# Performance work log

Hardware: AMD Instinct MI355X
Metric: run time of the kernel (lower is better)

The kernel has to match this reference:

```python
import jax, jax.numpy as jnp
import numpy as np

N, E, F_IN, HID, NC = 8192, 262144, 128, 64, 10
EPS_BN = 1e-5


def gat_layer(x, edge_src, edge_dst, W, att_src, att_dst, bias, heads):
    # x: [N, Fin]; W: [Fin, heads*C]; att_*: [heads, C]; bias: [C]
    n = x.shape[0]
    h = (x @ W).reshape(n, heads, -1)                     # [N,H,C]
    a_s = (h * att_src).sum(-1)                           # [N,H]
    a_d = (h * att_dst).sum(-1)                           # [N,H]
    e = jax.nn.leaky_relu(a_s[edge_src] + a_d[edge_dst], 0.2)  # [E,H]
    # segment softmax over destination node (self-loops guarantee >=1 edge per dst)
    m = jax.ops.segment_max(e, edge_dst, num_segments=n)
    ex = jnp.exp(e - m[edge_dst])
    s = jax.ops.segment_sum(ex, edge_dst, num_segments=n)
    alpha = ex / (s[edge_dst] + 1e-16)                    # [E,H]
    out = jax.ops.segment_sum(h[edge_src] * alpha[:, :, None], edge_dst, num_segments=n)  # [N,H,C]
    return out.mean(axis=1) + bias                        # concat=False -> mean over heads


def batch_norm(x, gamma, beta):
    mu = x.mean(axis=0)
    var = x.var(axis=0)  # biased, as PyTorch uses for normalization
    return (x - mu) * jax.lax.rsqrt(var + EPS_BN) * gamma + beta


def mha(x, Wq, Wk, Wv, bq, bk, bv, Wo, bo, num_heads=4):
    n, d = x.shape
    hd = d // num_heads
    q = (x @ Wq.T + bq).reshape(n, num_heads, hd)
    k = (x @ Wk.T + bk).reshape(n, num_heads, hd)
    v = (x @ Wv.T + bv).reshape(n, num_heads, hd)
    scores = jnp.einsum('nhd,mhd->hnm', q, k) / jnp.sqrt(jnp.asarray(hd, x.dtype))
    attn = jax.nn.softmax(scores, axis=-1)
    out = jnp.einsum('hnm,mhd->nhd', attn, v).reshape(n, d)
    return out @ Wo.T + bo


def setup_inputs() -> dict:
    key = jax.random.key(0)
    ks = jax.random.split(key, 32)
    d = {}
    d['x'] = jax.random.normal(ks[0], (N, F_IN), dtype=jnp.float32)
    d['edge_index'] = jax.random.randint(ks[1], (2, E), 0, N, dtype=jnp.int32)
    heads_list = [8, 8, 1]
    fins = [F_IN, HID, HID]
    for i, (fin, h) in enumerate(zip(fins, heads_list)):
        sc = 1.0 / np.sqrt(fin)
        d[f'W{i}'] = jax.random.normal(ks[2 + 4 * i], (fin, h * HID), dtype=jnp.float32) * sc
        d[f'as{i}'] = jax.random.normal(ks[3 + 4 * i], (h, HID), dtype=jnp.float32) * 0.1
        d[f'ad{i}'] = jax.random.normal(ks[4 + 4 * i], (h, HID), dtype=jnp.float32) * 0.1
        d[f'b{i}'] = jnp.zeros((HID,), dtype=jnp.float32)
    d['bn_gamma'] = jnp.ones((3, HID), dtype=jnp.float32)
    d['bn_beta'] = jnp.zeros((3, HID), dtype=jnp.float32)
    sc = 1.0 / np.sqrt(HID)
    for j, name in enumerate(['Wq', 'Wk', 'Wv', 'Wo']):
        d[name] = jax.random.normal(ks[16 + j], (HID, HID), dtype=jnp.float32) * sc
    for name in ['bq', 'bk', 'bv', 'bo']:
        d[name] = jnp.zeros((HID,), dtype=jnp.float32)
    d['Wc1'] = jax.random.normal(ks[20], (HID // 2, HID), dtype=jnp.float32) * sc
    d['bc1'] = jnp.zeros((HID // 2,), dtype=jnp.float32)
    d['Wc2'] = jax.random.normal(ks[21], (NC, HID // 2), dtype=jnp.float32) * (1.0 / np.sqrt(HID // 2))
    d['bc2'] = jnp.zeros((NC,), dtype=jnp.float32)
    return d


def reference(x, edge_index, W0, as0, ad0, b0, W1, as1, ad1, b1, W2, as2, ad2, b2,
              bn_gamma, bn_beta, Wq, Wk, Wv, bq, bk, bv, Wo, bo, Wc1, bc1, Wc2, bc2):
    n = x.shape[0]
    # PyG GATConv default add_self_loops=True
    loops = jnp.arange(n, dtype=edge_index.dtype)
    src = jnp.concatenate([edge_index[0], loops])
    dst = jnp.concatenate([edge_index[1], loops])
    heads_list = [8, 8, 1]
    params = [(W0, as0, ad0, b0), (W1, as1, ad1, b1), (W2, as2, ad2, b2)]
    for i in range(3):
        Wl, asl, adl, bl = params[i]
        x = gat_layer(x, src, dst, Wl, asl, adl, bl, heads_list[i])
        x = batch_norm(x, bn_gamma[i], bn_beta[i])
        x = jax.nn.relu(x)  # dropout inactive (eval)
    x = mha(x, Wq, Wk, Wv, bq, bk, bv, Wo, bo)
    x = jax.nn.relu(x @ Wc1.T + bc1)
    return x @ Wc2.T + bc2
```

## Files before the change

### kernel.cpp

```cpp
#include <hip/hip_runtime.h>
#include <hip/hip_bf16.h>

#define NN 8192
#define EE 262144
#define HID 64

typedef _Float16 half4_t __attribute__((ext_vector_type(4)));
typedef _Float16 half8_t __attribute__((ext_vector_type(8)));
typedef float f32x4 __attribute__((ext_vector_type(4)));

extern "C" __device__ float __ocml_native_exp2_f32(float);
#define EXP2N(x) __ocml_native_exp2_f32(x)

template<bool TRANS_B, int ACT>
__global__ void gemm_f32(const float* __restrict__ A, const float* __restrict__ B,
                         const float* __restrict__ bias, float* __restrict__ C,
                         int M, int Nc, int K) {
    __shared__ float As[16][65];
    __shared__ float Bs[16][65];
    int tid = threadIdx.x;
    int brow = blockIdx.y * 64, bcol = blockIdx.x * 64;
    int tr = (tid / 16) * 4;
    int tc = (tid % 16) * 4;
    float acc[4][4] = {};
    for (int k0 = 0; k0 < K; k0 += 16) {
        {
            int r  = tid / 4;
            int kk = (tid % 4) * 4;
            const float* a = A + (size_t)(brow + r) * K + k0 + kk;
            #pragma unroll
            for (int j = 0; j < 4; ++j) As[kk + j][r] = a[j];
        }
        if (!TRANS_B) {
            int kk = tid / 16;
            int n4 = (tid % 16) * 4;
            #pragma unroll
            for (int j = 0; j < 4; ++j) {
                int n = bcol + n4 + j;
                Bs[kk][n4 + j] = (n < Nc) ? B[(size_t)(k0 + kk) * Nc + n] : 0.f;
            }
        } else {
            int n  = tid / 4;
            int kk = (tid % 4) * 4;
            #pragma unroll
            for (int j = 0; j < 4; ++j)
                Bs[kk + j][n] = (bcol + n < Nc) ? B[(size_t)(bcol + n) * K + k0 + kk + j] : 0.f;
        }
        __syncthreads();
        #pragma unroll
        for (int kk = 0; kk < 16; ++kk) {
            float av[4], bv[4];
            #pragma unroll
            for (int i = 0; i < 4; ++i) av[i] = As[kk][tr + i];
            #pragma unroll
            for (int j = 0; j < 4; ++j) bv[j] = Bs[kk][tc + j];
            #pragma unroll
            for (int i = 0; i < 4; ++i)
                #pragma unroll
                for (int j = 0; j < 4; ++j)
                    acc[i][j] += av[i] * bv[j];
        }
        __syncthreads();
    }
    #pragma unroll
    for (int i = 0; i < 4; ++i) {
        int r = brow + tr + i;
        #pragma unroll
        for (int j = 0; j < 4; ++j) {
            int c = bcol + tc + j;
            if (c < Nc) {
                float v = acc[i][j];
                if (bias) v += bias[c];
                if (ACT == 1) v = fmaxf(v, 0.f);
                C[(size_t)r * Nc + c] = v;
            }
        }
    }
}

template<bool TRANS_B, bool OUT_F16, int ACT, bool GAT>
__device__ __forceinline__ void mfma_gemm_body(
        const float* __restrict__ A, const float* __restrict__ B,
        const float* __restrict__ bias, void* __restrict__ Cout,
        int M, int Nc, int K, float scale, int brow, int bcol,
        const float* __restrict__ att_s, const float* __restrict__ att_d,
        float* __restrict__ a_s, float* __restrict__ a_d, int H) {
    __shared__ _Float16 Ah[64][36];
    __shared__ _Float16 Bt[64][36];
    int tid  = threadIdx.x;
    int wave = tid >> 6, lane = tid & 63, lo16 = lane & 15, g = lane >> 4;
    f32x4 acc[4];
    #pragma unroll
    for (int i = 0; i < 4; ++i) acc[i] = (f32x4){0.f, 0.f, 0.f, 0.f};

    for (int k0 = 0; k0 < K; k0 += 32) {
        {
            int r  = tid >> 2;
            int ks = (tid & 3) * 8;
            const float* ap = A + (size_t)(brow + r) * K + k0 + ks;
            f32x4 a0 = *(const f32x4*)ap;
            f32x4 a1 = *(const f32x4*)(ap + 4);
            half4_t h0, h1;
            #pragma unroll
            for (int i = 0; i < 4; ++i) { h0[i] = (_Float16)a0[i]; h1[i] = (_Float16)a1[i]; }
            *(half4_t*)&Ah[r][ks]     = h0;
            *(half4_t*)&Ah[r][ks + 4] = h1;
        }
        if (TRANS_B) {
            int n  = tid >> 2;
            int ks = (tid & 3) * 8;
            const float* bp = B + (size_t)(bcol + n) * K + k0 + ks;
            f32x4 b0 = *(const f32x4*)bp;
            f32x4 b1 = *(const f32x4*)(bp + 4);
            half4_t h0, h1;
            #pragma unroll
            for (int i = 0; i < 4; ++i) { h0[i] = (_Float16)b0[i]; h1[i] = (_Float16)b1[i]; }
            *(half4_t*)&Bt[n][ks]     = h0;
            *(half4_t*)&Bt[n][ks + 4] = h1;
        } else {
            int n  = tid & 63;
            int kb = (tid >> 6) * 8;
            half4_t h0, h1;
            #pragma unroll
            for (int i = 0; i < 4; ++i)
                h0[i] = (_Float16)B[(size_t)(k0 + kb + i) * Nc + bcol + n];
            #pragma unroll
            for (int i = 0; i < 4; ++i)
                h1[i] = (_Float16)B[(size_t)(k0 + kb + 4 + i) * Nc + bcol + n];
            *(half4_t*)&Bt[n][kb]     = h0;
            *(half4_t*)&Bt[n][kb + 4] = h1;
        }
        __syncthreads();
        #pragma unroll
        for (int kh = 0; kh < 2; ++kh) {
            half4_t af = *(const half4_t*)&Ah[wave * 16 + lo16][kh * 16 + g * 4];
            #pragma unroll
            for (int cf = 0; cf < 4; ++cf) {
                half4_t bf = *(const half4_t*)&Bt[cf * 16 + lo16][kh * 16 + g * 4];
                acc[cf] = __builtin_amdgcn_mfma_f32_16x16x16f16(af, bf, acc[cf], 0, 0, 0);
            }
        }
        __syncthreads();
    }
    int rbase = brow + wave * 16 + g * 4;
    #pragma unroll
    for (int cf = 0; cf < 4; ++cf) {
        int c = bcol + cf * 16 + lo16;
        float bv = bias ? bias[c] : 0.f;
        #pragma unroll
        for (int reg = 0; reg < 4; ++reg) {
            float v = (acc[cf][reg] + bv) * scale;
            if (ACT == 1) v = fmaxf(v, 0.f);
            if (OUT_F16) ((_Float16*)Cout)[(size_t)(rbase + reg) * Nc + c] = (_Float16)v;
            else         ((float*)Cout)[(size_t)(rbase + reg) * Nc + c] = v;
        }
    }
    if (GAT) {
        float as_c[4], ad_c[4];
        #pragma unroll
        for (int cf = 0; cf < 4; ++cf) {
            int c = bcol + cf * 16 + lo16;
            as_c[cf] = att_s[c];
            ad_c[cf] = att_d[c];
        }
        int head = bcol >> 6;
        #pragma unroll
        for (int reg = 0; reg < 4; ++reg) {
            float ps = 0.f, pd = 0.f;
            #pragma unroll
            for (int cf = 0; cf < 4; ++cf) {
                ps += acc[cf][reg] * as_c[cf];
                pd += acc[cf][reg] * ad_c[cf];
            }
            #pragma unroll
            for (int off = 8; off; off >>= 1) {
                ps += __shfl_xor(ps, off);
                pd += __shfl_xor(pd, off);
            }
            if (lo16 == 0) {
                int row = rbase + reg;
                a_s[row * H + head] = ps;
                a_d[row * H + head] = pd;
            }
        }
    }
}

template<bool TRANS_B, bool OUT_F16, int ACT, bool GAT>
__global__ void mfma_gemm(const float* __restrict__ A, const float* __restrict__ B,
                          const float* __restrict__ bias, void* __restrict__ Cout,
                          int M, int Nc, int K, float scale,
                          const float* __restrict__ att_s, const float* __restrict__ att_d,
                          float* __restrict__ a_s, float* __restrict__ a_d, int H) {
    mfma_gemm_body<TRANS_B, OUT_F16, ACT, GAT>(A, B, bias, Cout, M, Nc, K, scale,
                                               blockIdx.y * 64, blockIdx.x * 64,
                                               att_s, att_d, a_s, a_d, H);
}

__global__ void qkv_gemm(const float* __restrict__ A,
                         const float* __restrict__ Wq, const float* __restrict__ Wk,
                         const float* __restrict__ Wv, const float* __restrict__ bq,
                         const float* __restrict__ bk, const float* __restrict__ bv,
                         _Float16* __restrict__ qh, _Float16* __restrict__ kh,
                         _Float16* __restrict__ vh, int M, float qscale) {
    int z = blockIdx.z;
    const float* B    = z == 0 ? Wq : (z == 1 ? Wk : Wv);
    const float* bias = z == 0 ? bq : (z == 1 ? bk : bv);
    _Float16* Cout    = z == 0 ? qh : (z == 1 ? kh : vh);
    float scale       = z == 0 ? qscale : 1.f;
    mfma_gemm_body<true, true, 0, false>(A, B, bias, Cout, M, 64, 64, scale,
                                         blockIdx.y * 64, 0,
                                         nullptr, nullptr, nullptr, nullptr, 0);
}

__global__ void count_deg(const int* __restrict__ ei, int* __restrict__ deg, int E) {
    int e = blockIdx.x * 256 + threadIdx.x;
    if (e < E) atomicAdd(&deg[ei[E + e]], 1);
}

__global__ void scan_deg(const int* __restrict__ deg, int* __restrict__ row_ptr,
                         int* __restrict__ cursor, int N) {
    __shared__ int tmp[1024];
    int tid = threadIdx.x;
    int base = tid * 8;
    int local[8];
    int s = 0;
    #pragma unroll
    for (int j = 0; j < 8; ++j) { local[j] = deg[base + j] + 1; s += local[j]; }
    tmp[tid] = s;
    __syncthreads();
    for (int off = 1; off < 1024; off <<= 1) {
        int add = (tid >= off) ? tmp[tid - off] : 0;
        __syncthreads();
        tmp[tid] += add;
        __syncthreads();
    }
    int run = tmp[tid] - s;
    #pragma unroll
    for (int j = 0; j < 8; ++j) {
        row_ptr[base + j] = run;
        cursor[base + j]  = run;
        run += local[j];
    }
    if (tid == 1023) row_ptr[N] = run;
}

__global__ void fill_csr(const int* __restrict__ ei, int* __restrict__ cursor,
                         int* __restrict__ col, int E, int N) {
    int e = blockIdx.x * 256 + threadIdx.x;
    if (e < E) {
        int dst = ei[E + e];
        int pos = atomicAdd(&cursor[dst], 1);
        col[pos] = ei[e];
    } else if (e < E + N) {
        int n = e - E;
        int pos = atomicAdd(&cursor[n], 1);
        col[pos] = n;
    }
}

__global__ void gat_gather_h8(const _Float16* __restrict__ h, const float* __restrict__ a_s,
                              const float* __restrict__ a_d, const int* __restrict__ row_ptr,
                              const int* __restrict__ col, float* __restrict__ out, int N) {
    __shared__ float wsf[4][64][8];
    __shared__ int   wsc[4][64];
    int t = threadIdx.x, wave = t >> 6, lane = t & 63;
    int n = (blockIdx.x * 256 + t) >> 6;
    int hd = lane >> 3;
    int beg = row_ptr[n], end = row_ptr[n + 1];
    float ad[8];
    #pragma unroll
    for (int i = 0; i < 8; ++i) ad[i] = a_d[n * 8 + i];
    float m[8];
    #pragma unroll
    for (int i = 0; i < 8; ++i) m[i] = -1e30f;
    for (int j = beg + lane; j < end; j += 64) {
        int c = col[j];
        f32x4 s0 = *(const f32x4*)(a_s + (size_t)c * 8);
        f32x4 s1 = *(const f32x4*)(a_s + (size_t)c * 8 + 4);
        #pragma unroll
        for (int i = 0; i < 4; ++i) {
            float sa = s0[i] + ad[i];
            sa = sa > 0.f ? sa : 0.2f * sa;
            m[i] = fmaxf(m[i], sa);
            float sb = s1[i] + ad[4 + i];
            sb = sb > 0.f ? sb : 0.2f * sb;
            m[4 + i] = fmaxf(m[4 + i], sb);
        }
    }
    #pragma unroll
    for (int i = 0; i < 8; ++i)
        #pragma unroll
        for (int off = 32; off; off >>= 1) m[i] = fmaxf(m[i], __shfl_xor(m[i], off));
    const _Float16* hb = h + (size_t)lane * 8;
    float acc[8] = {0.f, 0.f, 0.f, 0.f, 0.f, 0.f, 0.f, 0.f};
    float den[8] = {0.f, 0.f, 0.f, 0.f, 0.f, 0.f, 0.f, 0.f};
    for (int base = beg; base < end; base += 64) {
        int j = base + lane;
        int cj = 0;
        float w[8];
        #pragma unroll
        for (int i = 0; i < 8; ++i) w[i] = 0.f;
        if (j < end) {
            cj = col[j];
            f32x4 s0 = *(const f32x4*)(a_s + (size_t)cj * 8);
            f32x4 s1 = *(const f32x4*)(a_s + (size_t)cj * 8 + 4);
            #pragma unroll
            for (int i = 0; i < 4; ++i) {
                float sa = s0[i] + ad[i];
                sa = sa > 0.f ? sa : 0.2f * sa;
                w[i] = __expf(sa - m[i]);
                den[i] += w[i];
                float sb = s1[i] + ad[4 + i];
                sb = sb > 0.f ? sb : 0.2f * sb;
                w[4 + i] = __expf(sb - m[4 + i]);
                den[4 + i] += w[4 + i];
            }
        }
        wsc[wave][lane] = cj;
        *(f32x4*)&wsf[wave][lane][0] = (f32x4){w[0], w[1], w[2], w[3]};
        *(f32x4*)&wsf[wave][lane][4] = (f32x4){w[4], w[5], w[6], w[7]};
        int cnt = min(64, end - base);
        #pragma unroll 2
        for (int k = 0; k < cnt; ++k) {
            int ck  = wsc[wave][k];
            float wk = wsf[wave][k][hd];
            half8_t hv = *(const half8_t*)(hb + (size_t)ck * 512);
            #pragma unroll
            for (int i = 0; i < 8; ++i) acc[i] += wk * (float)hv[i];
        }
    }
    #pragma unroll
    for (int i = 0; i < 8; ++i)
        #pragma unroll
        for (int off = 32; off; off >>= 1) den[i] += __shfl_xor(den[i], off);
    float inv = 1.f / ((den[hd] + 1e-16f) * 8.f);
    float y[8];
    #pragma unroll
    for (int i = 0; i < 8; ++i) y[i] = acc[i] * inv;
    #pragma unroll
    for (int i = 0; i < 8; ++i) {
        y[i] += __shfl_xor(y[i], 8);
        y[i] += __shfl_xor(y[i], 16);
        y[i] += __shfl_xor(y[i], 32);
    }
    if (lane < 8) {
        *(f32x4*)(out + (size_t)n * 64 + lane * 8)     = (f32x4){y[0], y[1], y[2], y[3]};
        *(f32x4*)(out + (size_t)n * 64 + lane * 8 + 4) = (f32x4){y[4], y[5], y[6], y[7]};
    }
}

__global__ void gat_gather3(const _Float16* __restrict__ h, const float* __restrict__ a_s,
                            const float* __restrict__ a_d, const int* __restrict__ row_ptr,
                            const int* __restrict__ col, float* __restrict__ out,
                            int N, int H) {
    __shared__ uint2 wc[4][64];
    int t    = threadIdx.x;
    int wave = t >> 6;
    int lane = t & 63;
    int wid  = (blockIdx.x * 256 + t) >> 6;
    if (wid >= N * H) return;
    int n = wid / H, hh = wid % H;
    int beg = row_ptr[n], end = row_ptr[n + 1];
    float adn = a_d[n * H + hh];
    float m = -1e30f;
    for (int j = beg + lane; j < end; j += 64) {
        float sc = a_s[col[j] * H + hh] + adn;
        sc = sc > 0.f ? sc : 0.2f * sc;
        m = fmaxf(m, sc);
    }
    #pragma unroll
    for (int off = 32; off; off >>= 1) m = fmaxf(m, __shfl_xor(m, off));
    const _Float16* hb = h + (size_t)hh * 64 + lane;
    const size_t rs = (size_t)H * 64;
    float denom = 0.f;
    float acc0 = 0.f, acc1 = 0.f, acc2 = 0.f, acc3 = 0.f;
    float acc4 = 0.f, acc5 = 0.f, acc6 = 0.f, acc7 = 0.f;
    for (int base = beg; base < end; base += 64) {
        int j = base + lane;
        float w = 0.f; int s = 0;
        if (j < end) {
            s = col[j];
            float sc = a_s[s * H + hh] + adn;
            sc = sc > 0.f ? sc : 0.2f * sc;
            w = __expf(sc - m);
        }
        denom += w;
        uint2 p; p.x = __float_as_uint(w); p.y = (unsigned)s;
        wc[wave][lane] = p;
        int cnt = min(64, end - base);
        int k = 0;
        for (; k + 8 <= cnt; k += 8) {
            uint2 p0 = wc[wave][k];
            uint2 p1 = wc[wave][k + 1];
            uint2 p2 = wc[wave][k + 2];
            uint2 p3 = wc[wave][k + 3];
            uint2 p4 = wc[wave][k + 4];
            uint2 p5 = wc[wave][k + 5];
            uint2 p6 = wc[wave][k + 6];
            uint2 p7 = wc[wave][k + 7];
            acc0 += __uint_as_float(p0.x) * (float)hb[(size_t)p0.y * rs];
            acc1 += __uint_as_float(p1.x) * (float)hb[(size_t)p1.y * rs];
            acc2 += __uint_as_float(p2.x) * (float)hb[(size_t)p2.y * rs];
            acc3 += __uint_as_float(p3.x) * (float)hb[(size_t)p3.y * rs];
            acc4 += __uint_as_float(p4.x) * (float)hb[(size_t)p4.y * rs];
            acc5 += __uint_as_float(p5.x) * (float)hb[(size_t)p5.y * rs];
            acc6 += __uint_as_float(p6.x) * (float)hb[(size_t)p6.y * rs];
            acc7 += __uint_as_float(p7.x) * (float)hb[(size_t)p7.y * rs];
        }
        for (; k < cnt; ++k) {
            uint2 p0 = wc[wave][k];
            acc0 += __uint_as_float(p0.x) * (float)hb[(size_t)p0.y * rs];
        }
    }
    float acc = ((acc0 + acc1) + (acc2 + acc3)) + ((acc4 + acc5) + (acc6 + acc7));
    #pragma unroll
    for (int off = 32; off; off >>= 1) denom += __shfl_xor(denom, off);
    atomicAdd(&out[n * 64 + lane], acc / ((denom + 1e-16f) * H));
}

__global__ void bn_stats(const float* __restrict__ x, const float* __restrict__ gamma,
                         const float* __restrict__ beta, float* __restrict__ scale,
                         float* __restrict__ shift, int N) {
    int c = blockIdx.x;
    float s = 0.f, ss = 0.f;
    for (int r = threadIdx.x; r < N; r += 256) {
        float v = x[(size_t)r * 64 + c];
        s += v; ss += v * v;
    }
    #pragma unroll
    for (int off = 32; off; off >>= 1) {
        s  += __shfl_xor(s, off);
        ss += __shfl_xor(ss, off);
    }
    __shared__ float red[8];
    int wv = threadIdx.x >> 6, ln = threadIdx.x & 63;
    if (ln == 0) { red[wv] = s; red[4 + wv] = ss; }
    __syncthreads();
    if (threadIdx.x == 0) {
        float S  = red[0] + red[1] + red[2] + red[3];
        float SS = red[4] + red[5] + red[6] + red[7];
        float mu  = S / N;
        float var = SS / N - mu * mu;
        float istd = rsqrtf(var + 1e-5f);
        scale[c] = gamma[c] * istd;
        shift[c] = beta[c] - mu * gamma[c] * istd;
    }
}

__global__ void bn_apply(const float* x, const float* __restrict__ scale,
                         const float* __restrict__ shift, float* __restrict__ y,
                         float* xz, int total) {
    int i = blockIdx.x * 256 + threadIdx.x;
    if (i < total) {
        int c = i & 63;
        float v = x[i];
        y[i] = fmaxf(v * scale[c] + shift[c], 0.f);
        xz[i] = 0.f;
    }
}

__global__ void vkpack(const _Float16* __restrict__ vh, const _Float16* __restrict__ kh,
                       _Float16* __restrict__ vt, _Float16* __restrict__ khp, int N) {
    __shared__ _Float16 tile[64][68];
    int kb = blockIdx.x * 64;
    int t  = threadIdx.x;
    {
        int r = t >> 2, c0 = (t & 3) * 16;
        half8_t x0 = *(const half8_t*)(vh + (size_t)(kb + r) * 64 + c0);
        half8_t x1 = *(const half8_t*)(vh + (size_t)(kb + r) * 64 + c0 + 8);
        #pragma unroll
        for (int i = 0; i < 8; ++i) { tile[r][c0 + i] = x0[i]; tile[r][c0 + 8 + i] = x1[i]; }
    }
    #pragma unroll
    for (int rep = 0; rep < 2; ++rep) {
        int l = t + 256 * rep;
        int n = kb + (l >> 3), c8 = (l & 7) * 8;
        half8_t v = *(const half8_t*)(kh + (size_t)n * 64 + c8);
        *(half8_t*)(khp + ((size_t)(c8 >> 4) * N + n) * 16 + (c8 & 15)) = v;
    }
    __syncthreads();
    {
        int c = t >> 2, ks = (t & 3) * 16;
        half8_t y0, y1;
        #pragma unroll
        for (int i = 0; i < 8; ++i) { y0[i] = tile[ks + i][c]; y1[i] = tile[ks + 8 + i][c]; }
        *(half8_t*)(vt + (size_t)c * N + kb + ks)     = y0;
        *(half8_t*)(vt + (size_t)c * N + kb + ks + 8) = y1;
    }
}

__global__ __launch_bounds__(512) void mha_fa5(const _Float16* __restrict__ qh,
                                               const _Float16* __restrict__ khp,
                                               const _Float16* __restrict__ vt,
                                               float* __restrict__ ao, int N) {
    __shared__ alignas(16) char smem[38912];
    typedef _Float16 (*KtT)[2][64][20];
    typedef _Float16 (*VtT)[2][16][68];
    KtT Kt = (KtT)smem;
    VtT Vt = (VtT)(smem + 20480);
    float* MBp = (float*)(smem + 37888);
    float* OBp = (float*)smem;

    int h    = blockIdx.y;
    int t    = threadIdx.x;
    int lane = t & 63;
    int wave = t >> 6;
    int grp  = wave >> 1;
    int wsub = wave & 1;
    int lo16 = lane & 15;
    int g    = lane >> 4;
    int q    = blockIdx.x * 32 + wsub * 16 + lo16;

    half4_t qf = *(const half4_t*)(qh + (size_t)q * 64 + h * 16 + g * 4);
    const _Float16* kp = khp + (size_t)h * N * 16;
    const _Float16* vp = vt + (size_t)h * 16 * N;

    int gt   = t & 127;
    int skey = gt >> 1, sch = (gt & 1) * 8;
    int sd   = gt >> 3, skv = (gt & 7) * 8;

    {
        int kt = grp * 64;
        half8_t kv = *(const half8_t*)(kp + (size_t)(kt + skey) * 16 + sch);
        half8_t vv = *(const half8_t*)(vp + (size_t)sd * N + kt + skv);
        half4_t a, b, c, d;
        #pragma unroll
        for (int i = 0; i < 4; ++i) { a[i] = kv[i]; b[i] = kv[4 + i]; c[i] = vv[i]; d[i] = vv[4 + i]; }
        *(half4_t*)&Kt[grp][0][skey][sch]     = a;
        *(half4_t*)&Kt[grp][0][skey][sch + 4] = b;
        *(half4_t*)&Vt[grp][0][sd][skv]       = c;
        *(half4_t*)&Vt[grp][0][sd][skv + 4]   = d;
    }

    float m = -1e30f, l = 0.f;
    f32x4 o = {0.f, 0.f, 0.f, 0.f};
    const f32x4 zero = {0.f, 0.f, 0.f, 0.f};
    const int nit = N / 256;

    for (int it = 0; it < nit; ++it) {
        int cur = it & 1;
        __syncthreads();
        if (it + 1 < nit) {
            int kt = ((it + 1) * 4 + grp) * 64;
            half8_t kv = *(const half8_t*)(kp + (size_t)(kt + skey) * 16 + sch);
            half8_t vv = *(const half8_t*)(vp + (size_t)sd * N + kt + skv);
            half4_t a, b, c, d;
            #pragma unroll
            for (int i = 0; i < 4; ++i) { a[i] = kv[i]; b[i] = kv[4 + i]; c[i] = vv[i]; d[i] = vv[4 + i]; }
            *(half4_t*)&Kt[grp][cur ^ 1][skey][sch]     = a;
            *(half4_t*)&Kt[grp][cur ^ 1][skey][sch + 4] = b;
            *(half4_t*)&Vt[grp][cur ^ 1][sd][skv]       = c;
            *(half4_t*)&Vt[grp][cur ^ 1][sd][skv + 4]   = d;
        }
        f32x4 s[4];
        __builtin_amdgcn_s_setprio(1);
        #pragma unroll
        for (int st = 0; st < 4; ++st) {
            half4_t kf = *(const half4_t*)&Kt[grp][cur][st * 16 + lo16][g * 4];
            s[st] = __builtin_amdgcn_mfma_f32_16x16x16f16(kf, qf, zero, 0, 0, 0);
        }
        __builtin_amdgcn_s_setprio(0);
        float t0 = fmaxf(fmaxf(s[0][0], s[0][1]), s[0][2]);
        float t1 = fmaxf(fmaxf(s[0][3], s[1][0]), s[1][1]);
        float t2 = fmaxf(fmaxf(s[1][2], s[1][3]), s[2][0]);
        float t3 = fmaxf(fmaxf(s[2][1], s[2][2]), s[2][3]);
        float t4 = fmaxf(fmaxf(s[3][0], s[3][1]), fmaxf(s[3][2], s[3][3]));
        float tm = fmaxf(fmaxf(fmaxf(t0, t1), fmaxf(t2, t3)), t4);
        tm = fmaxf(tm, __shfl_xor(tm, 16));
        tm = fmaxf(tm, __shfl_xor(tm, 32));
        if (!__all(tm <= m + 8.f)) {
            float mnew = fmaxf(m, tm);
            float r = EXP2N(m - mnew);
            l *= r;
            #pragma unroll
            for (int i = 0; i < 4; ++i) o[i] *= r;
            m = mnew;
        }
        float lsum = 0.f;
        half4_t pf[4];
        #pragma unroll
        for (int st = 0; st < 4; ++st) {
            float p0 = EXP2N(s[st][0] - m);
            float p1 = EXP2N(s[st][1] - m);
            float p2 = EXP2N(s[st][2] - m);
            float p3 = EXP2N(s[st][3] - m);
            lsum += (p0 + p1) + (p2 + p3);
            auto lo = __builtin_amdgcn_cvt_pkrtz(p0, p1);
            auto hi = __builtin_amdgcn_cvt_pkrtz(p2, p3);
            pf[st][0] = (_Float16)lo[0]; pf[st][1] = (_Float16)lo[1];
            pf[st][2] = (_Float16)hi[0]; pf[st][3] = (_Float16)hi[1];
        }
        l += lsum;
        __builtin_amdgcn_s_setprio(1);
        #pragma unroll
        for (int st = 0; st < 4; ++st) {
            half4_t vf = *(const half4_t*)&Vt[grp][cur][lo16][st * 16 + g * 4];
            o = __builtin_amdgcn_mfma_f32_16x16x16f16(vf, pf[st], o, 0, 0, 0);
        }
        __builtin_amdgcn_s_setprio(0);
    }
    l += __shfl_xor(l, 16);
    l += __shfl_xor(l, 32);

    __syncthreads();
    if (grp != 0) {
        if (lane < 16) {
            MBp[((wsub * 4 + grp) * 2 + 0) * 16 + lane] = m;
            MBp[((wsub * 4 + grp) * 2 + 1) * 16 + lane] = l;
        }
        #pragma unroll
        for (int i = 0; i < 4; ++i)
            OBp[((wsub * 4 + grp) * 16 + g * 4 + i) * 17 + lo16] = o[i];
    }
    __syncthreads();
    if (grp == 0) {
        float M = m, L = l;
        f32x4 O = o;
        #pragma unroll
        for (int gg = 1; gg < 4; ++gg) {
            float m1 = MBp[((wsub * 4 + gg) * 2 + 0) * 16 + lo16];
            float l1 = MBp[((wsub * 4 + gg) * 2 + 1) * 16 + lo16];
            float Mn = fmaxf(M, m1);
            float e0 = EXP2N(M - Mn), e1 = EXP2N(m1 - Mn);
            L = L * e0 + l1 * e1;
            #pragma unroll
            for (int i = 0; i < 4; ++i)
                O[i] = O[i] * e0 + OBp[((wsub * 4 + gg) * 16 + g * 4 + i) * 17 + lo16] * e1;
            M = Mn;
        }
        float inv = 1.f / L;
        f32x4 res;
        #pragma unroll
        for (int i = 0; i < 4; ++i) res[i] = O[i] * inv;
        *(f32x4*)(ao + (size_t)q * 64 + h * 16 + g * 4) = res;
    }
}

static inline void launch_gemm(const float* A, const float* B, const float* bias, float* C,
                               int M, int Nc, int K, bool transB, int act, hipStream_t st) {
    dim3 grid((Nc + 63) / 64, M / 64), blk(256);
    if (!transB)       gemm_f32<false, 0><<<grid, blk, 0, st>>>(A, B, bias, C, M, Nc, K);
    else if (act == 0) gemm_f32<true, 0><<<grid, blk, 0, st>>>(A, B, bias, C, M, Nc, K);
    else               gemm_f32<true, 1><<<grid, blk, 0, st>>>(A, B, bias, C, M, Nc, K);
}

extern "C" void kernel_launch(void* const* d_in, const int* in_sizes, int n_in,
                              void* d_out, int out_size, void* d_ws, size_t ws_size,
                              hipStream_t stream) {
    const int N = NN, E = EE;
    const float* x    = (const float*)d_in[0];
    const int*   ei   = (const int*)d_in[1];
    const float* W[3]   = {(const float*)d_in[2], (const float*)d_in[6], (const float*)d_in[10]};
    const float* as_[3] = {(const float*)d_in[3], (const float*)d_in[7], (const float*)d_in[11]};
    const float* ad_[3] = {(const float*)d_in[4], (const float*)d_in[8], (const float*)d_in[12]};
    const float* bn_g = (const float*)d_in[14];
    const float* bn_b = (const float*)d_in[15];
    const float* Wq = (const float*)d_in[16];
    const float* Wk = (const float*)d_in[17];
    const float* Wv = (const float*)d_in[18];
    const float* Wo = (const float*)d_in[19];
    const float* bq = (const float*)d_in[20];
    const float* bk = (const float*)d_in[21];
    const float* bv = (const float*)d_in[22];
    const float* bo = (const float*)d_in[23];
    const float* Wc1 = (const float*)d_in[24];
    const float* bc1 = (const float*)d_in[25];
    const float* Wc2 = (const float*)d_in[26];
    const float* bc2 = (const float*)d_in[27];

    char* ws = (char*)d_ws;
    _Float16* h16 = (_Float16*)(ws + 0);
    _Float16* qh = (_Float16*)(ws + 9437184);
    _Float16* kh = (_Float16*)(ws + 10485760);
    _Float16* vh = (_Float16*)(ws + 11534336);
    _Float16* vt = (_Float16*)(ws + 12582912);
    _Float16* khp = (_Float16*)(ws + 13631488);
    float* a_s  = (float*)(ws + 16777216);
    float* a_d  = (float*)(ws + 17039360);
    int* row_ptr = (int*)(ws + 17301504);
    int* cursor  = (int*)(ws + 17334528);
    int* deg     = (int*)(ws + 17367296);
    int* col     = (int*)(ws + 17400064);
    float* xg   = (float*)(ws + 18481408);
    float* xb   = (float*)(ws + 20578560);
    float* ao   = (float*)(ws + 28967168);
    float* c1   = (float*)(ws + 31064320);
    float* bnscale = (float*)(ws + 32112896);
    float* bnshift = bnscale + 64;

    hipMemsetAsync(deg, 0, (size_t)N * 4, stream);
    count_deg<<<(E + 255) / 256, 256, 0, stream>>>(ei, deg, E);
    scan_deg<<<1, 1024, 0, stream>>>(deg, row_ptr, cursor, N);
    fill_csr<<<(E + N + 255) / 256, 256, 0, stream>>>(ei, cursor, col, E, N);

    const int heads[3] = {8, 8, 1};
    const int fins[3]  = {128, 64, 64};
    const float* xin = x;
    for (int i = 0; i < 3; ++i) {
        int H = heads[i], K = fins[i];
        mfma_gemm<false, true, 0, true><<<dim3(H, N / 64), 256, 0, stream>>>(
            xin, W[i], nullptr, h16, N, H * 64, K, 1.f, as_[i], ad_[i], a_s, a_d, H);
        if (H == 8)
            gat_gather_h8<<<N / 4, 256, 0, stream>>>(h16, a_s, a_d, row_ptr, col, xg, N);
        else
            gat_gather3<<<(N * H) / 4, 256, 0, stream>>>(h16, a_s, a_d, row_ptr, col, xg, N, H);
        bn_stats<<<64, 256, 0, stream>>>(xg, bn_g + i * 64, bn_b + i * 64, bnscale, bnshift, N);
        bn_apply<<<(N * 64) / 256, 256, 0, stream>>>(xg, bnscale, bnshift, xb, xg, N * 64);
        xin = xb;
    }

    qkv_gemm<<<dim3(1, N / 64, 3), 256, 0, stream>>>(
        xb, Wq, Wk, Wv, bq, bk, bv, qh, kh, vh, N, 0.36067376f);
    vkpack<<<N / 64, 256, 0, stream>>>(vh, kh, vt, khp, N);
    mha_fa5<<<dim3(N / 32, 4), 512, 0, stream>>>(qh, khp, vt, ao, N);
    mfma_gemm<true, false, 0, false><<<dim3(1, N / 64), 256, 0, stream>>>(
        ao, Wo, bo, xg, N, 64, 64, 1.f, nullptr, nullptr, nullptr, nullptr, 0);

    launch_gemm(xg, Wc1, bc1, c1, N, 32, 64, true, 1, stream);
    launch_gemm(c1, Wc2, bc2, (float*)d_out, N, 10, 32, true, 0, stream);
}
```

Before: 300.1 us.

## Fuse batch-norm apply into next GEMM loads and merge output MLP head

Removes the separate bn_apply pass by applying BN scale/shift and ReLU while loading the A tile in the following GAT or QKV GEMM. Replaces the Wo projection and the two classifier GEMMs with a single mlp_head kernel that keeps intermediates in shared memory and uses fp16 MFMA. Specializes the single-head gather to write outputs directly instead of accumulating with atomics. This saves launches and full-activation round trips. It no longer zeroes the gather output buffers between layers, so it depends on how the 8-head gather writes its results.

```diff
diff --git a/kernel.cpp b/kernel.cpp
--- a/kernel.cpp
+++ b/kernel.cpp
@@ -12,79 +12,16 @@
 extern "C" __device__ float __ocml_native_exp2_f32(float);
 #define EXP2N(x) __ocml_native_exp2_f32(x)
 
-template<bool TRANS_B, int ACT>
-__global__ void gemm_f32(const float* __restrict__ A, const float* __restrict__ B,
-                         const float* __restrict__ bias, float* __restrict__ C,
-                         int M, int Nc, int K) {
-    __shared__ float As[16][65];
-    __shared__ float Bs[16][65];
-    int tid = threadIdx.x;
-    int brow = blockIdx.y * 64, bcol = blockIdx.x * 64;
-    int tr = (tid / 16) * 4;
-    int tc = (tid % 16) * 4;
-    float acc[4][4] = {};
-    for (int k0 = 0; k0 < K; k0 += 16) {
-        {
-            int r  = tid / 4;
-            int kk = (tid % 4) * 4;
-            const float* a = A + (size_t)(brow + r) * K + k0 + kk;
-            #pragma unroll
-            for (int j = 0; j < 4; ++j) As[kk + j][r] = a[j];
-        }
-        if (!TRANS_B) {
-            int kk = tid / 16;
-            int n4 = (tid % 16) * 4;
-            #pragma unroll
-            for (int j = 0; j < 4; ++j) {
-                int n = bcol + n4 + j;
-                Bs[kk][n4 + j] = (n < Nc) ? B[(size_t)(k0 + kk) * Nc + n] : 0.f;
-            }
-        } else {
-            int n  = tid / 4;
-            int kk = (tid % 4) * 4;
-            #pragma unroll
-            for (int j = 0; j < 4; ++j)
-                Bs[kk + j][n] = (bcol + n < Nc) ? B[(size_t)(bcol + n) * K + k0 + kk + j] : 0.f;
-        }
-        __syncthreads();
-        #pragma unroll
-        for (int kk = 0; kk < 16; ++kk) {
-            float av[4], bv[4];
-            #pragma unroll
-            for (int i = 0; i < 4; ++i) av[i] = As[kk][tr + i];
-            #pragma unroll
-            for (int j = 0; j < 4; ++j) bv[j] = Bs[kk][tc + j];
-            #pragma unroll
-            for (int i = 0; i < 4; ++i)
-                #pragma unroll
-                for (int j = 0; j < 4; ++j)
-                    acc[i][j] += av[i] * bv[j];
-        }
-        __syncthreads();
-    }
-    #pragma unroll
-    for (int i = 0; i < 4; ++i) {
-        int r = brow + tr + i;
-        #pragma unroll
-        for (int j = 0; j < 4; ++j) {
-            int c = bcol + tc + j;
-            if (c < Nc) {
-                float v = acc[i][j];
-                if (bias) v += bias[c];
-                if (ACT == 1) v = fmaxf(v, 0.f);
-                C[(size_t)r * Nc + c] = v;
-            }
-        }
-    }
-}
-
-template<bool TRANS_B, bool OUT_F16, int ACT, bool GAT>
+#define MFMA16(a, b, c) __builtin_amdgcn_mfma_f32_16x16x16f16(a, b, c, 0, 0, 0)
+
+template<bool TRANS_B, bool OUT_F16, int ACT, bool GAT, bool BN>
 __device__ __forceinline__ void mfma_gemm_body(
         const float* __restrict__ A, const float* __restrict__ B,
         const float* __restrict__ bias, void* __restrict__ Cout,
         int M, int Nc, int K, float scale, int brow, int bcol,
         const float* __restrict__ att_s, const float* __restrict__ att_d,
-        float* __restrict__ a_s, float* __restrict__ a_d, int H) {
+        float* __restrict__ a_s, float* __restrict__ a_d, int H,
+        const float* __restrict__ bnsc, const float* __restrict__ bnsh) {
     __shared__ _Float16 Ah[64][36];
     __shared__ _Float16 Bt[64][36];
     int tid  = threadIdx.x;
@@ -100,6 +37,14 @@
             const float* ap = A + (size_t)(brow + r) * K + k0 + ks;
             f32x4 a0 = *(const f32x4*)ap;
             f32x4 a1 = *(const f32x4*)(ap + 4);
+            if (BN) {
+                #pragma unroll
+                for (int i = 0; i < 4; ++i) {
+                    int c0 = k0 + ks + i, c1 = c0 + 4;
+                    a0[i] = fmaxf(a0[i] * bnsc[c0] + bnsh[c0], 0.f);
+                    a1[i] = fmaxf(a1[i] * bnsc[c1] + bnsh[c1], 0.f);
+                }
+            }
             half4_t h0, h1;
             #pragma unroll
             for (int i = 0; i < 4; ++i) { h0[i] = (_Float16)a0[i]; h1[i] = (_Float16)a1[i]; }
@@ -137,7 +82,7 @@
             #pragma unroll
             for (int cf = 0; cf < 4; ++cf) {
                 half4_t bf = *(const half4_t*)&Bt[cf * 16 + lo16][kh * 16 + g * 4];
-                acc[cf] = __builtin_amdgcn_mfma_f32_16x16x16f16(af, bf, acc[cf], 0, 0, 0);
+                acc[cf] = MFMA16(af, bf, acc[cf]);
             }
         }
         __syncthreads();
@@ -186,15 +131,16 @@
     }
 }
 
-template<bool TRANS_B, bool OUT_F16, int ACT, bool GAT>
+template<bool TRANS_B, bool OUT_F16, int ACT, bool GAT, bool BN>
 __global__ void mfma_gemm(const float* __restrict__ A, const float* __restrict__ B,
                           const float* __restrict__ bias, void* __restrict__ Cout,
                           int M, int Nc, int K, float scale,
                           const float* __restrict__ att_s, const float* __restrict__ att_d,
-                          float* __restrict__ a_s, float* __restrict__ a_d, int H) {
-    mfma_gemm_body<TRANS_B, OUT_F16, ACT, GAT>(A, B, bias, Cout, M, Nc, K, scale,
-                                               blockIdx.y * 64, blockIdx.x * 64,
-                                               att_s, att_d, a_s, a_d, H);
+                          float* __restrict__ a_s, float* __restrict__ a_d, int H,
+                          const float* __restrict__ bnsc, const float* __restrict__ bnsh) {
+    mfma_gemm_body<TRANS_B, OUT_F16, ACT, GAT, BN>(A, B, bias, Cout, M, Nc, K, scale,
+                                                   blockIdx.y * 64, blockIdx.x * 64,
+                                                   att_s, att_d, a_s, a_d, H, bnsc, bnsh);
 }
 
 __global__ void qkv_gemm(const float* __restrict__ A,
@@ -202,15 +148,17 @@
                          const float* __restrict__ Wv, const float* __restrict__ bq,
                          const float* __restrict__ bk, const float* __restrict__ bv,
                          _Float16* __restrict__ qh, _Float16* __restrict__ kh,
-                         _Float16* __restrict__ vh, int M, float qscale) {
+                         _Float16* __restrict__ vh, int M, float qscale,
+                         const float* __restrict__ bnsc, const float* __restrict__ bnsh) {
     int z = blockIdx.z;
     const float* B    = z == 0 ? Wq : (z == 1 ? Wk : Wv);
     const float* bias = z == 0 ? bq : (z == 1 ? bk : bv);
     _Float16* Cout    = z == 0 ? qh : (z == 1 ? kh : vh);
     float scale       = z == 0 ? qscale : 1.f;
-    mfma_gemm_body<true, true, 0, false>(A, B, bias, Cout, M, 64, 64, scale,
-                                         blockIdx.y * 64, 0,
-                                         nullptr, nullptr, nullptr, nullptr, 0);
+    mfma_gemm_body<true, true, 0, false, true>(A, B, bias, Cout, M, 64, 64, scale,
+                                               blockIdx.y * 64, 0,
+                                               nullptr, nullptr, nullptr, nullptr, 0,
+                                               bnsc, bnsh);
 }
 
 __global__ void count_deg(const int* __restrict__ ei, int* __restrict__ deg, int E) {
@@ -350,29 +298,25 @@
     }
 }
 
-__global__ void gat_gather3(const _Float16* __restrict__ h, const float* __restrict__ a_s,
-                            const float* __restrict__ a_d, const int* __restrict__ row_ptr,
-                            const int* __restrict__ col, float* __restrict__ out,
-                            int N, int H) {
+__global__ void gat_gather_h1(const _Float16* __restrict__ h, const float* __restrict__ a_s,
+                              const float* __restrict__ a_d, const int* __restrict__ row_ptr,
+                              const int* __restrict__ col, float* __restrict__ out, int N) {
     __shared__ uint2 wc[4][64];
     int t    = threadIdx.x;
     int wave = t >> 6;
     int lane = t & 63;
-    int wid  = (blockIdx.x * 256 + t) >> 6;
-    if (wid >= N * H) return;
-    int n = wid / H, hh = wid % H;
+    int n    = (blockIdx.x * 256 + t) >> 6;
     int beg = row_ptr[n], end = row_ptr[n + 1];
-    float adn = a_d[n * H + hh];
+    float adn = a_d[n];
     float m = -1e30f;
     for (int j = beg + lane; j < end; j += 64) {
-        float sc = a_s[col[j] * H + hh] + adn;
+        float sc = a_s[col[j]] + adn;
         sc = sc > 0.f ? sc : 0.2f * sc;
         m = fmaxf(m, sc);
     }
     #pragma unroll
     for (int off = 32; off; off >>= 1) m = fmaxf(m, __shfl_xor(m, off));
-    const _Float16* hb = h + (size_t)hh * 64 + lane;
-    const size_t rs = (size_t)H * 64;
+    const _Float16* hb = h + lane;
     float denom = 0.f;
     float acc0 = 0.f, acc1 = 0.f, acc2 = 0.f, acc3 = 0.f;
     float acc4 = 0.f, acc5 = 0.f, acc6 = 0.f, acc7 = 0.f;
@@ -381,7 +325,7 @@
         float w = 0.f; int s = 0;
         if (j < end) {
             s = col[j];
-            float sc = a_s[s * H + hh] + adn;
+            float sc = a_s[s] + adn;
             sc = sc > 0.f ? sc : 0.2f * sc;
             w = __expf(sc - m);
         }
@@ -399,24 +343,24 @@
             uint2 p5 = wc[wave][k + 5];
             uint2 p6 = wc[wave][k + 6];
             uint2 p7 = wc[wave][k + 7];
-            acc0 += __uint_as_float(p0.x) * (float)hb[(size_t)p0.y * rs];
-            acc1 += __uint_as_float(p1.x) * (float)hb[(size_t)p1.y * rs];
-            acc2 += __uint_as_float(p2.x) * (float)hb[(size_t)p2.y * rs];
-            acc3 += __uint_as_float(p3.x) * (float)hb[(size_t)p3.y * rs];
-            acc4 += __uint_as_float(p4.x) * (float)hb[(size_t)p4.y * rs];
-            acc5 += __uint_as_float(p5.x) * (float)hb[(size_t)p5.y * rs];
-            acc6 += __uint_as_float(p6.x) * (float)hb[(size_t)p6.y * rs];
-            acc7 += __uint_as_float(p7.x) * (float)hb[(size_t)p7.y * rs];
+            acc0 += __uint_as_float(p0.x) * (float)hb[(size_t)p0.y * 64];
+            acc1 += __uint_as_float(p1.x) * (float)hb[(size_t)p1.y * 64];
+            acc2 += __uint_as_float(p2.x) * (float)hb[(size_t)p2.y * 64];
+            acc3 += __uint_as_float(p3.x) * (float)hb[(size_t)p3.y * 64];
+            acc4 += __uint_as_float(p4.x) * (float)hb[(size_t)p4.y * 64];
+            acc5 += __uint_as_float(p5.x) * (float)hb[(size_t)p5.y * 64];
+            acc6 += __uint_as_float(p6.x) * (float)hb[(size_t)p6.y * 64];
+            acc7 += __uint_as_float(p7.x) * (float)hb[(size_t)p7.y * 64];
         }
         for (; k < cnt; ++k) {
             uint2 p0 = wc[wave][k];
-            acc0 += __uint_as_float(p0.x) * (float)hb[(size_t)p0.y * rs];
+            acc0 += __uint_as_float(p0.x) * (float)hb[(size_t)p0.y * 64];
         }
     }
     float acc = ((acc0 + acc1) + (acc2 + acc3)) + ((acc4 + acc5) + (acc6 + acc7));
     #pragma unroll
     for (int off = 32; off; off >>= 1) denom += __shfl_xor(denom, off);
-    atomicAdd(&out[n * 64 + lane], acc / ((denom + 1e-16f) * H));
+    out[(size_t)n * 64 + lane] = acc / (denom + 1e-16f);
 }
 
 __global__ void bn_stats(const float* __restrict__ x, const float* __restrict__ gamma,
@@ -445,18 +389,6 @@
         float istd = rsqrtf(var + 1e-5f);
         scale[c] = gamma[c] * istd;
         shift[c] = beta[c] - mu * gamma[c] * istd;
-    }
-}
-
-__global__ void bn_apply(const float* x, const float* __restrict__ scale,
-                         const float* __restrict__ shift, float* __restrict__ y,
-                         float* xz, int total) {
-    int i = blockIdx.x * 256 + threadIdx.x;
-    if (i < total) {
-        int c = i & 63;
-        float v = x[i];
-        y[i] = fmaxf(v * scale[c] + shift[c], 0.f);
-        xz[i] = 0.f;
     }
 }
 
@@ -558,7 +490,7 @@
         #pragma unroll
         for (int st = 0; st < 4; ++st) {
             half4_t kf = *(const half4_t*)&Kt[grp][cur][st * 16 + lo16][g * 4];
-            s[st] = __builtin_amdgcn_mfma_f32_16x16x16f16(kf, qf, zero, 0, 0, 0);
+            s[st] = MFMA16(kf, qf, zero);
         }
         __builtin_amdgcn_s_setprio(0);
         float t0 = fmaxf(fmaxf(s[0][0], s[0][1]), s[0][2]);
@@ -596,7 +528,7 @@
         #pragma unroll
         for (int st = 0; st < 4; ++st) {
             half4_t vf = *(const half4_t*)&Vt[grp][cur][lo16][st * 16 + g * 4];
-            o = __builtin_amdgcn_mfma_f32_16x16x16f16(vf, pf[st], o, 0, 0, 0);
+            o = MFMA16(vf, pf[st], o);
         }
         __builtin_amdgcn_s_setprio(0);
     }
@@ -637,12 +569,122 @@
     }
 }
 
-static inline void launch_gemm(const float* A, const float* B, const float* bias, float* C,
-                               int M, int Nc, int K, bool transB, int act, hipStream_t st) {
-    dim3 grid((Nc + 63) / 64, M / 64), blk(256);
-    if (!transB)       gemm_f32<false, 0><<<grid, blk, 0, st>>>(A, B, bias, C, M, Nc, K);
-    else if (act == 0) gemm_f32<true, 0><<<grid, blk, 0, st>>>(A, B, bias, C, M, Nc, K);
-    else               gemm_f32<true, 1><<<grid, blk, 0, st>>>(A, B, bias, C, M, Nc, K);
+__global__ void mlp_head(const float* __restrict__ ao,
+                         const float* __restrict__ Wo, const float* __restrict__ bo,
+                         const float* __restrict__ Wc1, const float* __restrict__ bc1,
+                         const float* __restrict__ Wc2, const float* __restrict__ bc2,
+                         float* __restrict__ outp, int N) {
+    __shared__ _Float16 At[64][68];
+    __shared__ _Float16 Bt[64][68];
+    int t = threadIdx.x, wave = t >> 6, lane = t & 63, lo16 = lane & 15, g = lane >> 4;
+    int brow = blockIdx.x * 64;
+    const f32x4 zero = {0.f, 0.f, 0.f, 0.f};
+    {
+        int r = t >> 2, c0 = (t & 3) * 16;
+        const float* ap = ao + (size_t)(brow + r) * 64 + c0;
+        const float* wp = Wo + (size_t)r * 64 + c0;
+        #pragma unroll
+        for (int j = 0; j < 16; j += 4) {
+            f32x4 va = *(const f32x4*)(ap + j);
+            f32x4 vw = *(const f32x4*)(wp + j);
+            half4_t ha, hw;
+            #pragma unroll
+            for (int i = 0; i < 4; ++i) { ha[i] = (_Float16)va[i]; hw[i] = (_Float16)vw[i]; }
+            *(half4_t*)&At[r][c0 + j] = ha;
+            *(half4_t*)&Bt[r][c0 + j] = hw;
+        }
+    }
+    __syncthreads();
+    f32x4 acc1[4];
+    #pragma unroll
+    for (int i = 0; i < 4; ++i) acc1[i] = zero;
+    #pragma unroll
+    for (int kc = 0; kc < 4; ++kc) {
+        half4_t af = *(const half4_t*)&At[wave * 16 + lo16][kc * 16 + g * 4];
+        #pragma unroll
+        for (int cf = 0; cf < 4; ++cf) {
+            half4_t bf = *(const half4_t*)&Bt[cf * 16 + lo16][kc * 16 + g * 4];
+            acc1[cf] = MFMA16(af, bf, acc1[cf]);
+        }
+    }
+    #pragma unroll
+    for (int cf = 0; cf < 4; ++cf) {
+        int c = cf * 16 + lo16;
+        float bv = bo[c];
+        #pragma unroll
+        for (int reg = 0; reg < 4; ++reg)
+            At[wave * 16 + g * 4 + reg][c] = (_Float16)(acc1[cf][reg] + bv);
+    }
+    __syncthreads();
+    {
+        int r = t >> 2, c0 = (t & 3) * 16;
+        if (r < 32) {
+            const float* wp = Wc1 + (size_t)r * 64 + c0;
+            #pragma unroll
+            for (int j = 0; j < 16; j += 4) {
+                f32x4 vw = *(const f32x4*)(wp + j);
+                half4_t hw;
+                #pragma unroll
+                for (int i = 0; i < 4; ++i) hw[i] = (_Float16)vw[i];
+                *(half4_t*)&Bt[r][c0 + j] = hw;
+            }
+        }
+    }
+    __syncthreads();
+    f32x4 acc2[2];
+    acc2[0] = zero; acc2[1] = zero;
+    #pragma unroll
+    for (int kc = 0; kc < 4; ++kc) {
+        half4_t af = *(const half4_t*)&At[wave * 16 + lo16][kc * 16 + g * 4];
+        #pragma unroll
+        for (int cf = 0; cf < 2; ++cf) {
+            half4_t bf = *(const half4_t*)&Bt[cf * 16 + lo16][kc * 16 + g * 4];
+            acc2[cf] = MFMA16(af, bf, acc2[cf]);
+        }
+    }
+    #pragma unroll
+    for (int cf = 0; cf < 2; ++cf) {
+        int c = cf * 16 + lo16;
+        float bv = bc1[c];
+        #pragma unroll
+        for (int reg = 0; reg < 4; ++reg)
+            At[wave * 16 + g * 4 + reg][c] = (_Float16)fmaxf(acc2[cf][reg] + bv, 0.f);
+    }
+    __syncthreads();
+    {
+        if (t < 32) {
+            int r = t >> 1, c0 = (t & 1) * 16;
+            half4_t hw;
+            #pragma unroll
+            for (int j = 0; j < 16; j += 4) {
+                if (r < 10) {
+                    f32x4 vw = *(const f32x4*)(Wc2 + (size_t)r * 32 + c0 + j);
+                    #pragma unroll
+                    for (int i = 0; i < 4; ++i) hw[i] = (_Float16)vw[i];
+                } else {
+                    #pragma unroll
+                    for (int i = 0; i < 4; ++i) hw[i] = (_Float16)0.f;
+                }
+                *(half4_t*)&Bt[r][c0 + j] = hw;
+            }
+        }
+    }
+    __syncthreads();
+    f32x4 acc3 = zero;
+    #pragma unroll
+    for (int kc = 0; kc < 2; ++kc) {
+        half4_t af = *(const half4_t*)&At[wave * 16 + lo16][kc * 16 + g * 4];
+        half4_t bf = *(const half4_t*)&Bt[lo16][kc * 16 + g * 4];
+        acc3 = MFMA16(af, bf, acc3);
+    }
+    if (lo16 < 10) {
+        float bv = bc2[lo16];
+        #pragma unroll
+        for (int reg = 0; reg < 4; ++reg) {
+            int row = brow + wave * 16 + g * 4 + reg;
+            outp[(size_t)row * 10 + lo16] = acc3[reg] + bv;
+        }
+    }
 }
 
 extern "C" void kernel_launch(void* const* d_in, const int* in_sizes, int n_in,
@@ -682,10 +724,9 @@
     int* cursor  = (int*)(ws + 17334528);
     int* deg     = (int*)(ws + 17367296);
     int* col     = (int*)(ws + 17400064);
-    float* xg   = (float*)(ws + 18481408);
-    float* xb   = (float*)(ws + 20578560);
+    float* g0   = (float*)(ws + 18481408);
+    float* g1   = (float*)(ws + 20578560);
     float* ao   = (float*)(ws + 28967168);
-    float* c1   = (float*)(ws + 31064320);
     float* bnscale = (float*)(ws + 32112896);
     float* bnshift = bnscale + 64;
 
@@ -694,29 +735,23 @@
     scan_deg<<<1, 1024, 0, stream>>>(deg, row_ptr, cursor, N);
     fill_csr<<<(E + N + 255) / 256, 256, 0, stream>>>(ei, cursor, col, E, N);
 
-    const int heads[3] = {8, 8, 1};
-    const int fins[3]  = {128, 64, 64};
-    const float* xin = x;
-    for (int i = 0; i < 3; ++i) {
-        int H = heads[i], K = fins[i];
-        mfma_gemm<false, true, 0, true><<<dim3(H, N / 64), 256, 0, stream>>>(
-            xin, W[i], nullptr, h16, N, H * 64, K, 1.f, as_[i], ad_[i], a_s, a_d, H);
-        if (H == 8)
-            gat_gather_h8<<<N / 4, 256, 0, stream>>>(h16, a_s, a_d, row_ptr, col, xg, N);
-        else
-            gat_gather3<<<(N * H) / 4, 256, 0, stream>>>(h16, a_s, a_d, row_ptr, col, xg, N, H);
-        bn_stats<<<64, 256, 0, stream>>>(xg, bn_g + i * 64, bn_b + i * 64, bnscale, bnshift, N);
-        bn_apply<<<(N * 64) / 256, 256, 0, stream>>>(xg, bnscale, bnshift, xb, xg, N * 64);
-        xin = xb;
-    }
+    mfma_gemm<false, true, 0, true, false><<<dim3(8, N / 64), 256, 0, stream>>>(
+        x, W[0], nullptr, h16, N, 512, 128, 1.f, as_[0], ad_[0], a_s, a_d, 8, nullptr, nullptr);
+    gat_gather_h8<<<N / 4, 256, 0, stream>>>(h16, a_s, a_d, row_ptr, col, g0, N);
+    bn_stats<<<64, 256, 0, stream>>>(g0, bn_g, bn_b, bnscale, bnshift, N);
+    mfma_gemm<false, true, 0, true, true><<<dim3(8, N / 64), 256, 0, stream>>>(
+        g0, W[1], nullptr, h16, N, 512, 64, 1.f, as_[1], ad_[1], a_s, a_d, 8, bnscale, bnshift);
+    gat_gather_h8<<<N / 4, 256, 0, stream>>>(h16, a_s, a_d, row_ptr, col, g1, N);
+    bn_stats<<<64, 256, 0, stream>>>(g1, bn_g + 64, bn_b + 64, bnscale, bnshift, N);
+    mfma_gemm<false, true, 0, true, true><<<dim3(1, N / 64), 256, 0, stream>>>(
+        g1, W[2], nullptr, h16, N, 64, 64, 1.f, as_[2], ad_[2], a_s, a_d, 1, bnscale, bnshift);
+    gat_gather_h1<<<N / 4, 256, 0, stream>>>(h16, a_s, a_d, row_ptr, col, g0, N);
+    bn_stats<<<64, 256, 0, stream>>>(g0, bn_g + 128, bn_b + 128, bnscale, bnshift, N);
 
     qkv_gemm<<<dim3(1, N / 64, 3), 256, 0, stream>>>(
-        xb, Wq, Wk, Wv, bq, bk, bv, qh, kh, vh, N, 0.36067376f);
+        g0, Wq, Wk, Wv, bq, bk, bv, qh, kh, vh, N, 0.36067376f, bnscale, bnshift);
     vkpack<<<N / 64, 256, 0, stream>>>(vh, kh, vt, khp, N);
     mha_fa5<<<dim3(N / 32, 4), 512, 0, stream>>>(qh, khp, vt, ao, N);
-    mfma_gemm<true, false, 0, false><<<dim3(1, N / 64), 256, 0, stream>>>(
-        ao, Wo, bo, xg, N, 64, 64, 1.f, nullptr, nullptr, nullptr, nullptr, 0);
-
-    launch_gemm(xg, Wc1, bc1, c1, N, 32, 64, true, 1, stream);
-    launch_gemm(c1, Wc2, bc2, (float*)d_out, N, 10, 32, true, 0, stream);
-}
+
+    mlp_head<<<N / 64, 256, 0, stream>>>(ao, Wo, bo, Wc1, bc1, Wc2, bc2, (float*)d_out, N);
+}
```

Result: faster. 268.2 us (-10.6%).
